# Kernel optimization log

Hardware: AMD Instinct MI355X
Metric: run time of the kernel (lower is better)

## Reference

```python
import jax, jax.numpy as jnp
import numpy as np
from jax import lax

B = 256
L = 1024
C = 64           # num_inputs == num_channels[l]
NUM_LAYERS = 5
KERNEL = 3
HID = 256
NUM_STATIC = 32
OUT_DIM = 2
KQ = 24576
T_TEMP = 0.07
NUM_NEIGHBORS = 1
EPS = 1e-12


def _l2n(x, axis):
    n = jnp.linalg.norm(x, axis=axis, keepdims=True)
    return x / jnp.maximum(n, EPS)


def _causal_conv(x, w, b, dil):
    # x: [B, C, L], w: [O, I, K] -> left-pad (K-1)*dil == Conv1d(pad both)+Chomp1d
    y = lax.conv_general_dilated(x, w, window_strides=(1,),
                                 padding=[((KERNEL - 1) * dil, 0)],
                                 rhs_dilation=(dil,),
                                 dimension_numbers=('NCH', 'OIH', 'NCH'))
    return y + b[None, :, None]


def _tcn(x, c1w, c1b, c2w, c2b):
    # stacked TemporalBlocks, dilation 2**l, identity residual (in==out channels)
    for l in range(NUM_LAYERS):
        d = 2 ** l
        h = jax.nn.relu(_causal_conv(x, c1w[l], c1b[l], d))
        h = jax.nn.relu(_causal_conv(h, c2w[l], c2b[l], d))
        x = jax.nn.relu(h + x)
    return x


def _mlp(x, w1, b1, w2, b2):
    # Linear -> ReLU -> Linear (use_batch_norm=False, eval: no dropout)
    return jax.nn.relu(x @ w1 + b1) @ w2 + b2


def setup_inputs() -> dict:
    key = jax.random.key(0)
    ks = jax.random.split(key, 24)
    d = {}
    d['sequence_q_s'] = jax.random.normal(ks[0], (B, L, C), jnp.float32)
    d['sequence_k_s'] = jax.random.normal(ks[1], (B, L, C), jnp.float32)
    d['static_s'] = jax.random.normal(ks[2], (B, NUM_STATIC), jnp.float32)
    d['sequence_q_t'] = jax.random.normal(ks[3], (B, L, C), jnp.float32)
    d['sequence_k_t'] = jax.random.normal(ks[4], (B, L, C), jnp.float32)
    d['static_t'] = jax.random.normal(ks[5], (B, NUM_STATIC), jnp.float32)
    d['alpha'] = jnp.ones((1,), jnp.float32)
    cs = 1.0 / np.sqrt(C * KERNEL)
    d['c1w'] = jax.random.normal(ks[6], (NUM_LAYERS, C, C, KERNEL), jnp.float32) * cs
    d['c1b'] = jnp.zeros((NUM_LAYERS, C), jnp.float32)
    d['c2w'] = jax.random.normal(ks[7], (NUM_LAYERS, C, C, KERNEL), jnp.float32) * cs
    d['c2b'] = jnp.zeros((NUM_LAYERS, C), jnp.float32)
    d['pjw1'] = jax.random.normal(ks[8], (C, HID), jnp.float32) / np.sqrt(C)
    d['pjb1'] = jnp.zeros((HID,), jnp.float32)
    d['pjw2'] = jax.random.normal(ks[9], (HID, C), jnp.float32) / np.sqrt(HID)
    d['pjb2'] = jnp.zeros((C,), jnp.float32)
    d['prw1'] = jax.random.normal(ks[10], (C + NUM_STATIC, HID), jnp.float32) / np.sqrt(C + NUM_STATIC)
    d['prb1'] = jnp.zeros((HID,), jnp.float32)
    d['prw2'] = jax.random.normal(ks[11], (HID, OUT_DIM), jnp.float32) / np.sqrt(HID)
    d['prb2'] = jnp.zeros((OUT_DIM,), jnp.float32)
    d['dw1'] = jax.random.normal(ks[12], (C, HID), jnp.float32) / np.sqrt(C)
    d['db1'] = jnp.zeros((HID,), jnp.float32)
    d['dw2'] = jax.random.normal(ks[13], (HID, 1), jnp.float32) / np.sqrt(HID)
    d['db2'] = jnp.zeros((1,), jnp.float32)
    qs = jax.random.normal(ks[14], (C, KQ), jnp.float32)
    qt = jax.random.normal(ks[15], (C, KQ), jnp.float32)
    d['queue_s'] = _l2n(qs, 0)
    d['queue_t'] = _l2n(qt, 0)
    return d


def reference(sequence_q_s, sequence_k_s, static_s, sequence_q_t, sequence_k_t, static_t, alpha,
              c1w, c1b, c2w, c2b, pjw1, pjb1, pjw2, pjb2, prw1, prb1, prw2, prb2,
              dw1, db1, dw2, db2, queue_s, queue_t):
    sg = lax.stop_gradient

    def encode(seq):  # [B, L, C] -> normalized [B, C]
        return _l2n(_tcn(jnp.transpose(seq, (0, 2, 1)), c1w, c1b, c2w, c2b)[:, :, -1], 1)

    q_s = encode(sequence_q_s)
    p_q_s = _l2n(_mlp(q_s, pjw1, pjb1, pjw2, pjb2), 1)
    q_t = encode(sequence_q_t)
    p_q_t = _l2n(_mlp(q_t, pjw1, pjb1, pjw2, pjb2), 1)
    # key encoder under no_grad (params equal to query encoder at init)
    k_s = sg(encode(sequence_k_s))
    k_t = sg(encode(sequence_k_t))

    logits_s = jnp.concatenate([p_q_s @ k_s.T, p_q_s @ sg(queue_s)], axis=1) / T_TEMP
    labels_s = jnp.arange(B, dtype=jnp.int32)
    logits_t = jnp.concatenate([p_q_t @ k_t.T, p_q_t @ sg(queue_t)], axis=1) / T_TEMP
    labels_t = jnp.arange(B, dtype=jnp.int32)

    # NN(k_t, q_s.detach()): cdist + topk smallest -> pseudo labels
    q_s_det = sg(q_s)
    d2 = (jnp.sum(k_t * k_t, 1)[:, None] + jnp.sum(q_s_det * q_s_det, 1)[None, :]
          - 2.0 * (k_t @ q_s_det.T))  # [B_t, B_s]
    _, idx = lax.top_k(-d2, NUM_NEIGHBORS)
    labels_ts = idx[:, 0]

    logits_ts = (q_t @ q_s_det.T) / T_TEMP

    labels_domain = jnp.concatenate([jnp.ones((B, 1), jnp.float32), jnp.zeros((B, 1), jnp.float32)], 0)
    # gradient reversal is identity in forward
    q_rev = jnp.concatenate([q_s, q_t], axis=0)
    pred_domain = _mlp(q_rev, dw1, db1, dw2, db2)

    y_s = _mlp(jnp.concatenate([q_s, static_s], axis=1), prw1, prb1, prw2, prb2)

    return (logits_s, labels_s, logits_t, labels_t, logits_ts, labels_ts,
            pred_domain, labels_domain, y_s)
```

## Files before the change

kernel.cpp:

```cpp
#include <hip/hip_runtime.h>
#include <hip/hip_bf16.h>

#define B_SZ   256
#define L_SZ   1024
#define C_SZ   64
#define HID    256
#define KQ     24576
#define WIN    125
#define WSTART (L_SZ - WIN)

#define OFF_LOGITS_S   0LL
#define OFF_LABELS_S   6356992LL
#define OFF_LOGITS_T   6357248LL
#define OFF_LABELS_T   12714240LL
#define OFF_LOGITS_TS  12714496LL
#define OFF_LABELS_TS  12780032LL
#define OFF_PRED_DOM   12780288LL
#define OFF_LABELS_DOM 12780800LL
#define OFF_YS         12781312LL

#define INV_T (1.0f / 0.07f)

typedef __attribute__((ext_vector_type(8))) short  bf16x8;
typedef __attribute__((ext_vector_type(4))) float  floatx4;
typedef __attribute__((ext_vector_type(16))) float floatx16;
typedef __attribute__((ext_vector_type(4))) unsigned short ushortx4;

__device__ __forceinline__ unsigned short f2bf_rne(float x) {
    unsigned u = __float_as_uint(x);
    unsigned r = u + 0x7fffu + ((u >> 16) & 1u);
    return (unsigned short)(r >> 16);
}
__device__ __forceinline__ float bf2f(unsigned short h) {
    return __uint_as_float(((unsigned)h) << 16);
}

__device__ __forceinline__ int swz2(int r) { return ((r >> 1) & 7) << 4; }

__device__ __forceinline__ bf16x8 dpp_tap1(bf16x8 f0, bf16x8 f2) {
    union U { bf16x8 v; int d[4]; } a, b, r;
    a.v = f0; b.v = f2;
#pragma unroll
    for (int k = 0; k < 4; ++k) {
        int patch = __builtin_amdgcn_update_dpp(0, b.d[k], 0x111, 0xf, 0xf, false);
        r.d[k]    = __builtin_amdgcn_update_dpp(patch, a.d[k], 0x101, 0xf, 0xf, false);
    }
    return r.v;
}

__global__ void prep_frag_kernel(const float* __restrict__ c1w,
                                 const float* __restrict__ c2w,
                                 unsigned short* __restrict__ wf) {
    int bid = blockIdx.x;
    int kb = bid & 1, mt = (bid >> 1) & 3;
    int sttap = bid >> 3;
    int tap = sttap % 3, st = sttap / 3;
    int l = st >> 1, cv = st & 1;
    int tid = threadIdx.x;
    int j = tid & 7, lane = tid >> 3;
    int co = mt * 16 + (lane & 15);
    int ci = kb * 32 + (lane >> 4) * 8 + j;
    const float* src = cv ? c2w : c1w;
    float w = src[((l * 64 + co) * 64 + ci) * 3 + tap];
    unsigned short hi = f2bf_rne(w);
    unsigned short lo = f2bf_rne(w - bf2f(hi));
    size_t b0 = ((((size_t)((st * 3 + tap) * 2 + 0)) * 4 + mt) * 2 + kb) * 512 + lane * 8 + j;
    size_t b1 = ((((size_t)((st * 3 + tap) * 2 + 1)) * 4 + mt) * 2 + kb) * 512 + lane * 8 + j;
    wf[b0] = hi;
    wf[b1] = lo;
}

#define R0H 0
#define R0L 16384
#define R1H 32768
#define R1L 40960
#define HHB 49152
#define HLB 65536
#define SCRATCH_B 57344

__device__ __forceinline__ void loadA(bf16x8 A[3][2][2], const bf16x8* __restrict__ wf8,
                                      int st, int mt, int lane) {
#pragma unroll
    for (int tap = 0; tap < 3; ++tap)
#pragma unroll
        for (int h = 0; h < 2; ++h)
#pragma unroll
            for (int kb = 0; kb < 2; ++kb)
                A[tap][h][kb] = wf8[((((st * 3 + tap) * 2 + h) * 4 + mt) * 2 + kb) * 64 + lane];
}

__device__ __forceinline__ void copyA(bf16x8 D[3][2][2], const bf16x8 S[3][2][2]) {
#pragma unroll
    for (int tap = 0; tap < 3; ++tap)
#pragma unroll
        for (int h = 0; h < 2; ++h)
#pragma unroll
            for (int kb = 0; kb < 2; ++kb)
                D[tap][h][kb] = S[tap][h][kb];
}

template<int TILES, bool RES, bool FINAL, bool DPP1>
__device__ __forceinline__ void conv_pass(
    char* lds, const bf16x8 A[3][2][2],
    int inH, int inL, int rows_valid, int stride,
    int outH, int outL, int n_out,
    int resH, int resL, int res_valid,
    const float* __restrict__ bias,
    int mt, int lg, int li)
{
    int co0 = mt * 16 + lg * 4;
    float4 b4 = *(const float4*)(bias + co0);
    float ba[4] = {b4.x, b4.y, b4.z, b4.w};

#pragma unroll
    for (int tt = 0; tt < TILES; ++tt) {
        int i = tt * 16 + li;
        floatx4 acc = {0.f, 0.f, 0.f, 0.f};
        if (DPP1) {
            int jr0 = i;       jr0 = (jr0 < rows_valid - 1) ? jr0 : (rows_valid - 1);
            int jr2 = i + 2;   jr2 = (jr2 < rows_valid - 1) ? jr2 : (rows_valid - 1);
            int sw0 = swz2(jr0), sw2 = swz2(jr2);
#pragma unroll
            for (int kb = 0; kb < 2; ++kb) {
                int cbase = kb * 64 + lg * 16;
                bf16x8 bH0 = *(const bf16x8*)(lds + inH + jr0 * 128 + (cbase ^ sw0));
                bf16x8 bL0 = *(const bf16x8*)(lds + inL + jr0 * 128 + (cbase ^ sw0));
                bf16x8 bH2 = *(const bf16x8*)(lds + inH + jr2 * 128 + (cbase ^ sw2));
                bf16x8 bL2 = *(const bf16x8*)(lds + inL + jr2 * 128 + (cbase ^ sw2));
                bf16x8 bH1 = dpp_tap1(bH0, bH2);
                bf16x8 bL1 = dpp_tap1(bL0, bL2);
                acc = __builtin_amdgcn_mfma_f32_16x16x32_bf16(A[0][0][kb], bH0, acc, 0, 0, 0);
                acc = __builtin_amdgcn_mfma_f32_16x16x32_bf16(A[0][0][kb], bL0, acc, 0, 0, 0);
                acc = __builtin_amdgcn_mfma_f32_16x16x32_bf16(A[0][1][kb], bH0, acc, 0, 0, 0);
                acc = __builtin_amdgcn_mfma_f32_16x16x32_bf16(A[1][0][kb], bH1, acc, 0, 0, 0);
                acc = __builtin_amdgcn_mfma_f32_16x16x32_bf16(A[1][0][kb], bL1, acc, 0, 0, 0);
                acc = __builtin_amdgcn_mfma_f32_16x16x32_bf16(A[1][1][kb], bH1, acc, 0, 0, 0);
                acc = __builtin_amdgcn_mfma_f32_16x16x32_bf16(A[2][0][kb], bH2, acc, 0, 0, 0);
                acc = __builtin_amdgcn_mfma_f32_16x16x32_bf16(A[2][0][kb], bL2, acc, 0, 0, 0);
                acc = __builtin_amdgcn_mfma_f32_16x16x32_bf16(A[2][1][kb], bH2, acc, 0, 0, 0);
            }
        } else {
#pragma unroll
            for (int tap = 0; tap < 3; ++tap) {
                int jr = i * stride + tap;
                jr = (jr < rows_valid - 1) ? jr : (rows_valid - 1);
                int sw = swz2(jr);
                const char* pH = lds + inH + jr * 128;
                const char* pL = lds + inL + jr * 128;
#pragma unroll
                for (int kb = 0; kb < 2; ++kb) {
                    int cb = (kb * 64 + lg * 16) ^ sw;
                    bf16x8 bH = *(const bf16x8*)(pH + cb);
                    bf16x8 bL = *(const bf16x8*)(pL + cb);
                    acc = __builtin_amdgcn_mfma_f32_16x16x32_bf16(A[tap][0][kb], bH, acc, 0, 0, 0);
                    acc = __builtin_amdgcn_mfma_f32_16x16x32_bf16(A[tap][0][kb], bL, acc, 0, 0, 0);
                    acc = __builtin_amdgcn_mfma_f32_16x16x32_bf16(A[tap][1][kb], bH, acc, 0, 0, 0);
                }
            }
        }
        float v[4];
#pragma unroll
        for (int r = 0; r < 4; ++r) v[r] = fmaxf(acc[r] + ba[r], 0.f);
        if (RES) {
            int rr = 2 * i + 4;
            rr = (rr < res_valid - 1) ? rr : (res_valid - 1);
            int rsw = swz2(rr);
            int rcb = (mt * 32 + lg * 8) ^ rsw;
            ushortx4 rh = *(const ushortx4*)(lds + resH + rr * 128 + rcb);
            ushortx4 rl = *(const ushortx4*)(lds + resL + rr * 128 + rcb);
#pragma unroll
            for (int r = 0; r < 4; ++r)
                v[r] = fmaxf(v[r] + bf2f(rh[r]) + bf2f(rl[r]), 0.f);
        }
        if (FINAL) {
            if (i == 0) {
                float* scratch = (float*)(lds + SCRATCH_B);
#pragma unroll
                for (int r = 0; r < 4; ++r) scratch[co0 + r] = v[r];
            }
        } else {
            if (i < n_out) {
                ushortx4 h4, l4;
#pragma unroll
                for (int r = 0; r < 4; ++r) {
                    unsigned short hh = f2bf_rne(v[r]);
                    h4[r] = (short)hh;
                    l4[r] = (short)f2bf_rne(v[r] - bf2f(hh));
                }
                int wsw = swz2(i);
                int wcb = (mt * 32 + lg * 8) ^ wsw;
                *(ushortx4*)(lds + outH + i * 128 + wcb) = h4;
                *(ushortx4*)(lds + outL + i * 128 + wcb) = l4;
            }
        }
    }
}

__launch_bounds__(256)
__global__ void encode_kernel(const float* __restrict__ sqs, const float* __restrict__ sks,
                              const float* __restrict__ sqt, const float* __restrict__ skt,
                              const unsigned short* __restrict__ wf,
                              const float* __restrict__ c1b, const float* __restrict__ c2b,
                              const float* __restrict__ pjw1, const float* __restrict__ pjb1,
                              const float* __restrict__ pjw2, const float* __restrict__ pjb2,
                              float* __restrict__ enc, float* __restrict__ proj,
                              unsigned short* __restrict__ pbf) {
    __shared__ char lds[81920];
    int b = blockIdx.x;
    int s = blockIdx.y;
    const float* seq = (s == 0) ? sqs : (s == 1) ? sks : (s == 2) ? sqt : skt;
    const float4* base4 = reinterpret_cast<const float4*>(seq + ((size_t)b * L_SZ + WSTART) * C_SZ);
    int tid = threadIdx.x;

    int mt   = tid >> 6;
    int lane = tid & 63;
    int lg = lane >> 4, li = lane & 15;
    const bf16x8* wf8 = (const bf16x8*)wf;

    bf16x8 A[3][2][2], An[3][2][2];
    loadA(A, wf8, 0, mt, lane);

    for (int idx = tid; idx < 2000; idx += 256) {
        float4 v = base4[idx];
        int t = idx >> 4, c0 = (idx & 15) * 4;
        int cb = (c0 * 2) ^ swz2(t);
        float vv[4] = {v.x, v.y, v.z, v.w};
        ushortx4 h4, l4;
#pragma unroll
        for (int r = 0; r < 4; ++r) {
            unsigned short hh = f2bf_rne(vv[r]);
            h4[r] = (short)hh;
            l4[r] = (short)f2bf_rne(vv[r] - bf2f(hh));
        }
        *(ushortx4*)(lds + R0H + t * 128 + cb) = h4;
        *(ushortx4*)(lds + R0L + t * 128 + cb) = l4;
    }
    __syncthreads();

    loadA(An, wf8, 1, mt, lane);
    conv_pass<8, false, false, true>(lds, A, R0H, R0L, 125, 1, HHB, HLB, 123, 0, 0, 0,
                                     c1b + 0, mt, lg, li);
    __syncthreads();
    copyA(A, An); loadA(An, wf8, 2, mt, lane);
    conv_pass<4, true, false, false>(lds, A, HHB, HLB, 123, 2, R1H, R1L, 61, R0H, R0L, 125,
                                     c2b + 0, mt, lg, li);
    __syncthreads();
    copyA(A, An);
    loadA(An, wf8, 3, mt, lane);
    conv_pass<4, false, false, true>(lds, A, R1H, R1L, 61, 1, HHB, HLB, 59, 0, 0, 0,
                                     c1b + 64, mt, lg, li);
    __syncthreads();
    copyA(A, An); loadA(An, wf8, 4, mt, lane);
    conv_pass<2, true, false, false>(lds, A, HHB, HLB, 59, 2, R0H, R0L, 29, R1H, R1L, 61,
                                     c2b + 64, mt, lg, li);
    __syncthreads();
    copyA(A, An);
    loadA(An, wf8, 5, mt, lane);
    conv_pass<2, false, false, true>(lds, A, R0H, R0L, 29, 1, HHB, HLB, 27, 0, 0, 0,
                                     c1b + 128, mt, lg, li);
    __syncthreads();
    copyA(A, An); loadA(An, wf8, 6, mt, lane);
    conv_pass<1, true, false, false>(lds, A, HHB, HLB, 27, 2, R1H, R1L, 13, R0H, R0L, 29,
                                     c2b + 128, mt, lg, li);
    __syncthreads();
    copyA(A, An);
    loadA(An, wf8, 7, mt, lane);
    conv_pass<1, false, false, true>(lds, A, R1H, R1L, 13, 1, HHB, HLB, 11, 0, 0, 0,
                                     c1b + 192, mt, lg, li);
    __syncthreads();
    copyA(A, An); loadA(An, wf8, 8, mt, lane);
    conv_pass<1, true, false, false>(lds, A, HHB, HLB, 11, 2, R0H, R0L, 5, R1H, R1L, 13,
                                     c2b + 192, mt, lg, li);
    __syncthreads();
    copyA(A, An);
    loadA(An, wf8, 9, mt, lane);
    conv_pass<1, false, false, true>(lds, A, R0H, R0L, 5, 1, HHB, HLB, 3, 0, 0, 0,
                                     c1b + 256, mt, lg, li);
    __syncthreads();
    copyA(A, An);
    conv_pass<1, true, true, false>(lds, A, HHB, HLB, 3, 2, R1H, R1L, 1, R0H, R0L, 5,
                                    c2b + 256, mt, lg, li);
    __syncthreads();

    float* xn = (float*)(lds + R0H);
    if (tid < 64) {
        float vv = ((float*)(lds + SCRATCH_B))[tid];
        float sq = vv * vv;
#pragma unroll
        for (int off = 32; off; off >>= 1) sq += __shfl_xor(sq, off, 64);
        float norm = fmaxf(sqrtf(sq), 1e-12f);
        float nv = vv / norm;
        enc[((size_t)s * B_SZ + b) * 64 + tid] = nv;
        xn[tid] = nv;
    }
    __syncthreads();

    if (s == 0 || s == 2) {
        float* hv   = (float*)(lds + R1H);
        float* red4 = (float*)(lds + R1H + 1024);
        {
            float acc = pjb1[tid];
            const float* wcol = pjw1 + tid;
            for (int c = 0; c < 64; ++c) acc = fmaf(xn[c], wcol[c * 256], acc);
            hv[tid] = fmaxf(acc, 0.f);
        }
        __syncthreads();
        {
            int wv = tid >> 6, o = tid & 63;
            float acc = 0.f;
            const float* wcol = pjw2 + o;
            int j0 = wv * 64;
            for (int j = j0; j < j0 + 64; ++j) acc = fmaf(hv[j], wcol[j * 64], acc);
            red4[wv * 64 + o] = acc;
        }
        __syncthreads();
        if (tid < 64) {
            float o = pjb2[tid];
#pragma unroll
            for (int k = 0; k < 4; ++k) o += red4[k * 64 + tid];
            float sq = o * o;
#pragma unroll
            for (int off = 32; off; off >>= 1) sq += __shfl_xor(sq, off, 64);
            float norm = fmaxf(sqrtf(sq), 1e-12f);
            float pv = o / norm;
            int which = s >> 1;
            proj[((size_t)which * B_SZ + b) * 64 + tid] = pv;
            pbf[((size_t)which * B_SZ + b) * 64 + tid] = f2bf_rne(pv);
        }
    }
}

__launch_bounds__(512)
__global__ void qlogits_kernel(const float* __restrict__ proj,
                               const unsigned short* __restrict__ pbf,
                               const float* __restrict__ enc,
                               const float* __restrict__ queue_s, const float* __restrict__ queue_t,
                               const float* __restrict__ stat,
                               const float* __restrict__ dw1, const float* __restrict__ db1,
                               const float* __restrict__ dw2, const float* __restrict__ db2,
                               const float* __restrict__ prw1, const float* __restrict__ prb1,
                               const float* __restrict__ prw2, const float* __restrict__ prb2,
                               float* __restrict__ out) {
    __shared__ char lds[8448];
    int bx = blockIdx.x;
    int sz = blockIdx.y;
    int tid = threadIdx.x;
    long long outBase0 = (sz == 0) ? OFF_LOGITS_S : OFF_LOGITS_T;

    if (bx >= 392) {
        int hb = (bx - 392) + sz * 513;
        if (hb < 256) {
            __shared__ float kt[64];
            __shared__ float qt[64];
            __shared__ float swv[8];
            __shared__ int   swj[8];
            int i = hb;
            if (tid < 64) {
                kt[tid] = enc[((size_t)3 * B_SZ + i) * 64 + tid];
                qt[tid] = enc[((size_t)2 * B_SZ + i) * 64 + tid];
            }
            __syncthreads();
            float bv = 1e30f; int bj = 0x7fffffff;
            if (tid < 256) {
                int j = tid;
                const float* qs = enc + (size_t)j * 64;
                float dkt = 0.f, dqt = 0.f, qq = 0.f, kk = 0.f;
                for (int c = 0; c < 64; ++c) {
                    float v = qs[c];
                    dkt = fmaf(kt[c], v, dkt);
                    dqt = fmaf(qt[c], v, dqt);
                    qq  = fmaf(v, v, qq);
                    kk  = fmaf(kt[c], kt[c], kk);
                }
                out[OFF_LOGITS_TS + (long long)i * 256 + j] = dqt * INV_T;
                bv = kk + qq - 2.f * dkt;
                bj = j;
            }
#pragma unroll
            for (int off = 32; off; off >>= 1) {
                float ov = __shfl_xor(bv, off, 64);
                int   oj = __shfl_xor(bj, off, 64);
                if (ov < bv || (ov == bv && oj < bj)) { bv = ov; bj = oj; }
            }
            int w = tid >> 6;
            if ((tid & 63) == 0) { swv[w] = bv; swj[w] = bj; }
            __syncthreads();
            if (tid == 0) {
                float best = swv[0]; int bi = swj[0];
#pragma unroll
                for (int k = 1; k < 8; ++k)
                    if (swv[k] < best || (swv[k] == best && swj[k] < bi)) { best = swv[k]; bi = swj[k]; }
                out[OFF_LABELS_TS + i] = (float)bi;
            }
        } else if (hb < 768) {
            __shared__ float xv[64];
            __shared__ float red[256];
            int r = hb - 256;
            const float* x = enc + ((r < 256) ? ((size_t)0 * B_SZ + r) : ((size_t)2 * B_SZ + (r - 256))) * 64;
            if (tid < 64) xv[tid] = x[tid];
            __syncthreads();
            if (tid < 256) {
                float h = db1[tid];
                for (int c = 0; c < 64; ++c) h = fmaf(xv[c], dw1[c * 256 + tid], h);
                h = fmaxf(h, 0.f);
                red[tid] = h * dw2[tid];
            }
            __syncthreads();
            for (int s2 = 128; s2; s2 >>= 1) {
                if (tid < s2) red[tid] += red[tid + s2];
                __syncthreads();
            }
            if (tid == 0) out[OFF_PRED_DOM + r] = red[0] + db2[0];
        } else if (hb < 1024) {
            __shared__ float xv[96];
            __shared__ float red[256];
            __shared__ float hsave[256];
            int b = hb - 768;
            if (tid < 64)       xv[tid] = enc[(size_t)b * 64 + tid];
            else if (tid < 96)  xv[tid] = stat[(size_t)b * 32 + (tid - 64)];
            __syncthreads();
            if (tid < 256) {
                float h = prb1[tid];
                for (int c = 0; c < 96; ++c) h = fmaf(xv[c], prw1[c * 256 + tid], h);
                hsave[tid] = fmaxf(h, 0.f);
            }
            __syncthreads();
            for (int o = 0; o < 2; ++o) {
                if (tid < 256) red[tid] = hsave[tid] * prw2[tid * 2 + o];
                __syncthreads();
                for (int s2 = 128; s2; s2 >>= 1) {
                    if (tid < s2) red[tid] += red[tid + s2];
                    __syncthreads();
                }
                if (tid == 0) out[OFF_YS + (long long)b * 2 + o] = red[0] + prb2[o];
                __syncthreads();
            }
        } else {
            int t = (hb - 1024) * 512 + tid;
            if (t < 256) {
                out[OFF_LABELS_S + t] = (float)t;
                out[OFF_LABELS_T + t] = (float)t;
            }
            if (t < 512) out[OFF_LABELS_DOM + t] = (t < 256) ? 1.f : 0.f;
        }
        return;
    }

    if (bx >= 384) {
        float (*pt)[65] = (float(*)[65])lds;
        int rt = bx - 384;
        const float* p = proj + ((size_t)sz * B_SZ + rt * 32) * 64;
        for (int idx = tid; idx < 32 * 64; idx += 512) {
            pt[idx >> 6][idx & 63] = p[idx];
        }
        __syncthreads();
        if (tid < 256) {
            float acc[32];
#pragma unroll
            for (int r = 0; r < 32; ++r) acc[r] = 0.f;
            int j = tid;
            const float* k = enc + ((size_t)(sz == 0 ? 1 : 3) * B_SZ + j) * 64;
            for (int c = 0; c < 64; ++c) {
                float bv = k[c];
#pragma unroll
                for (int r = 0; r < 32; ++r) acc[r] = fmaf(pt[r][c], bv, acc[r]);
            }
#pragma unroll
            for (int r = 0; r < 32; ++r) {
                out[outBase0 + (long long)(rt * 32 + r) * 24832 + j] = acc[r] * INV_T;
            }
        }
        return;
    }

    int j0 = bx * 64;
    const float* q = (sz == 0 ? queue_s : queue_t);

    {
#pragma unroll
        for (int pass = 0; pass < 2; ++pass) {
            int idx = pass * 512 + tid;
            int c = idx >> 4, jj0 = (idx & 15) * 4;
            float4 v = *(const float4*)(q + (size_t)c * KQ + j0 + jj0);
            float vv[4] = {v.x, v.y, v.z, v.w};
#pragma unroll
            for (int r = 0; r < 4; ++r) {
                int jj = jj0 + r;
                *(unsigned short*)(lds + jj * 128 + ((c * 2) ^ ((jj & 7) << 4))) = f2bf_rne(vv[r]);
            }
        }
    }
    __syncthreads();

    int w = tid >> 6, lane = tid & 63;
    int r31 = lane & 31, hi = lane >> 5;
    int arow = w * 32 + r31;
    const bf16x8* pa = (const bf16x8*)(pbf + ((size_t)sz * B_SZ + arow) * 64);
    bf16x8 A[4];
#pragma unroll
    for (int ks = 0; ks < 4; ++ks)
        A[ks] = pa[ks * 2 + hi];
    long long outBase = outBase0 + 256 + j0;
#pragma unroll
    for (int ct = 0; ct < 2; ++ct) {
        int col = ct * 32 + r31;
        bf16x8 Bf[4];
#pragma unroll
        for (int ks = 0; ks < 4; ++ks)
            Bf[ks] = *(const bf16x8*)(lds + col * 128 + (((ks * 16 + hi * 8) * 2) ^ ((col & 7) << 4)));
        floatx16 acc;
#pragma unroll
        for (int r = 0; r < 16; ++r) acc[r] = 0.f;
#pragma unroll
        for (int ks = 0; ks < 4; ++ks)
            acc = __builtin_amdgcn_mfma_f32_32x32x16_bf16(A[ks], Bf[ks], acc, 0, 0, 0);
#pragma unroll
        for (int r = 0; r < 16; ++r) {
            int drow = (r & 3) + 8 * (r >> 2) + 4 * hi;
            out[outBase + (long long)(w * 32 + drow) * 24832 + ct * 32 + r31] = acc[r] * INV_T;
        }
    }
}

extern "C" void kernel_launch(void* const* d_in, const int* in_sizes, int n_in,
                              void* d_out, int out_size, void* d_ws, size_t ws_size,
                              hipStream_t stream) {
    const float* sqs    = (const float*)d_in[0];
    const float* sks    = (const float*)d_in[1];
    const float* stat_s = (const float*)d_in[2];
    const float* sqt    = (const float*)d_in[3];
    const float* skt    = (const float*)d_in[4];
    const float* c1w    = (const float*)d_in[7];
    const float* c1b    = (const float*)d_in[8];
    const float* c2w    = (const float*)d_in[9];
    const float* c2b    = (const float*)d_in[10];
    const float* pjw1   = (const float*)d_in[11];
    const float* pjb1   = (const float*)d_in[12];
    const float* pjw2   = (const float*)d_in[13];
    const float* pjb2   = (const float*)d_in[14];
    const float* prw1   = (const float*)d_in[15];
    const float* prb1   = (const float*)d_in[16];
    const float* prw2   = (const float*)d_in[17];
    const float* prb2   = (const float*)d_in[18];
    const float* dw1    = (const float*)d_in[19];
    const float* db1    = (const float*)d_in[20];
    const float* dw2    = (const float*)d_in[21];
    const float* db2    = (const float*)d_in[22];
    const float* queue_s = (const float*)d_in[23];
    const float* queue_t = (const float*)d_in[24];

    float* out = (float*)d_out;
    unsigned short* wf = (unsigned short*)d_ws;
    float* enc  = (float*)((char*)d_ws + 491520);
    float* proj = enc + 65536;
    unsigned short* pbf = (unsigned short*)(proj + 32768);

    prep_frag_kernel<<<240, 512, 0, stream>>>(c1w, c2w, wf);
    encode_kernel<<<dim3(256, 4), 256, 0, stream>>>(sqs, sks, sqt, skt, wf, c1b, c2b,
                                                    pjw1, pjb1, pjw2, pjb2, enc, proj, pbf);
    qlogits_kernel<<<dim3(905, 2), 512, 0, stream>>>(proj, pbf, enc, queue_s, queue_t,
                                                     stat_s, dw1, db1, dw2, db2,
                                                     prw1, prb1, prw2, prb2, out);
}
```

Measured before the change: 79.76 us.

## Encode key-source and query-target sequences in single bf16 within shared blocks

```diff
diff --git a/kernel.cpp b/kernel.cpp
--- a/kernel.cpp
+++ b/kernel.cpp
@@ -78,22 +78,30 @@
 #define HLB 65536
 #define SCRATCH_B 57344
 
-__device__ __forceinline__ void loadA(bf16x8 A[3][2][2], const bf16x8* __restrict__ wf8,
-                                      int st, int mt, int lane) {
+#define L_IT   39808
+#define L_X0   0
+#define L_R1   16000
+#define L_HH   23808
+#define L_SCR  39552
+
+template<int NH>
+__device__ __forceinline__ void loadAx(bf16x8 A[3][NH][2], const bf16x8* __restrict__ wf8,
+                                       int st, int mt, int lane) {
 #pragma unroll
     for (int tap = 0; tap < 3; ++tap)
 #pragma unroll
-        for (int h = 0; h < 2; ++h)
+        for (int h = 0; h < NH; ++h)
 #pragma unroll
             for (int kb = 0; kb < 2; ++kb)
                 A[tap][h][kb] = wf8[((((st * 3 + tap) * 2 + h) * 4 + mt) * 2 + kb) * 64 + lane];
 }
 
-__device__ __forceinline__ void copyA(bf16x8 D[3][2][2], const bf16x8 S[3][2][2]) {
+template<int NH>
+__device__ __forceinline__ void copyAx(bf16x8 D[3][NH][2], const bf16x8 S[3][NH][2]) {
 #pragma unroll
     for (int tap = 0; tap < 3; ++tap)
 #pragma unroll
-        for (int h = 0; h < 2; ++h)
+        for (int h = 0; h < NH; ++h)
 #pragma unroll
             for (int kb = 0; kb < 2; ++kb)
                 D[tap][h][kb] = S[tap][h][kb];
@@ -124,10 +132,10 @@
             for (int kb = 0; kb < 2; ++kb) {
                 int cbase = kb * 64 + lg * 16;
                 bf16x8 bH0 = *(const bf16x8*)(lds + inH + jr0 * 128 + (cbase ^ sw0));
+                bf16x8 bH2 = *(const bf16x8*)(lds + inH + jr2 * 128 + (cbase ^ sw2));
+                bf16x8 bH1 = dpp_tap1(bH0, bH2);
                 bf16x8 bL0 = *(const bf16x8*)(lds + inL + jr0 * 128 + (cbase ^ sw0));
-                bf16x8 bH2 = *(const bf16x8*)(lds + inH + jr2 * 128 + (cbase ^ sw2));
                 bf16x8 bL2 = *(const bf16x8*)(lds + inL + jr2 * 128 + (cbase ^ sw2));
-                bf16x8 bH1 = dpp_tap1(bH0, bH2);
                 bf16x8 bL1 = dpp_tap1(bL0, bL2);
                 acc = __builtin_amdgcn_mfma_f32_16x16x32_bf16(A[0][0][kb], bH0, acc, 0, 0, 0);
                 acc = __builtin_amdgcn_mfma_f32_16x16x32_bf16(A[0][0][kb], bL0, acc, 0, 0, 0);
@@ -164,8 +172,7 @@
         if (RES) {
             int rr = 2 * i + 4;
             rr = (rr < res_valid - 1) ? rr : (res_valid - 1);
-            int rsw = swz2(rr);
-            int rcb = (mt * 32 + lg * 8) ^ rsw;
+            int rcb = (mt * 32 + lg * 8) ^ swz2(rr);
             ushortx4 rh = *(const ushortx4*)(lds + resH + rr * 128 + rcb);
             ushortx4 rl = *(const ushortx4*)(lds + resL + rr * 128 + rcb);
 #pragma unroll
@@ -178,22 +185,239 @@
 #pragma unroll
                 for (int r = 0; r < 4; ++r) scratch[co0 + r] = v[r];
             }
-        } else {
-            if (i < n_out) {
-                ushortx4 h4, l4;
-#pragma unroll
-                for (int r = 0; r < 4; ++r) {
-                    unsigned short hh = f2bf_rne(v[r]);
-                    h4[r] = (short)hh;
-                    l4[r] = (short)f2bf_rne(v[r] - bf2f(hh));
+        } else if (i < n_out) {
+            int wcb = (mt * 32 + lg * 8) ^ swz2(i);
+            ushortx4 h4, l4;
+#pragma unroll
+            for (int r = 0; r < 4; ++r) {
+                h4[r] = f2bf_rne(v[r]);
+                l4[r] = f2bf_rne(v[r] - bf2f(h4[r]));
+            }
+            *(ushortx4*)(lds + outH + i * 128 + wcb) = h4;
+            *(ushortx4*)(lds + outL + i * 128 + wcb) = l4;
+        }
+    }
+}
+
+__device__ __forceinline__ void encode_body_heavy(
+    char* lds, const float* __restrict__ base,
+    const bf16x8* __restrict__ wf8,
+    const float* __restrict__ c1b, const float* __restrict__ c2b,
+    int tid, int mt, int lane, int lg, int li)
+{
+    const float4* base4 = reinterpret_cast<const float4*>(base);
+    bf16x8 A[3][2][2], An[3][2][2];
+    loadAx<2>(A, wf8, 0, mt, lane);
+
+    for (int idx = tid; idx < 2000; idx += 256) {
+        float4 v = base4[idx];
+        int t = idx >> 4, c0 = (idx & 15) * 4;
+        int cb = (c0 * 2) ^ swz2(t);
+        float vv[4] = {v.x, v.y, v.z, v.w};
+        ushortx4 h4, l4;
+#pragma unroll
+        for (int r = 0; r < 4; ++r) {
+            h4[r] = f2bf_rne(vv[r]);
+            l4[r] = f2bf_rne(vv[r] - bf2f(h4[r]));
+        }
+        *(ushortx4*)(lds + R0H + t * 128 + cb) = h4;
+        *(ushortx4*)(lds + R0L + t * 128 + cb) = l4;
+    }
+    __syncthreads();
+
+    loadAx<2>(An, wf8, 1, mt, lane);
+    conv_pass<8, false, false, true>(lds, A, R0H, R0L, 125, 1, HHB, HLB, 123, 0, 0, 0,
+                                     c1b + 0, mt, lg, li);
+    __syncthreads();
+    copyAx<2>(A, An); loadAx<2>(An, wf8, 2, mt, lane);
+    conv_pass<4, true, false, false>(lds, A, HHB, HLB, 123, 2, R1H, R1L, 61, R0H, R0L, 125,
+                                     c2b + 0, mt, lg, li);
+    __syncthreads();
+    copyAx<2>(A, An);
+    loadAx<2>(An, wf8, 3, mt, lane);
+    conv_pass<4, false, false, true>(lds, A, R1H, R1L, 61, 1, HHB, HLB, 59, 0, 0, 0,
+                                     c1b + 64, mt, lg, li);
+    __syncthreads();
+    copyAx<2>(A, An); loadAx<2>(An, wf8, 4, mt, lane);
+    conv_pass<2, true, false, false>(lds, A, HHB, HLB, 59, 2, R0H, R0L, 29, R1H, R1L, 61,
+                                     c2b + 64, mt, lg, li);
+    __syncthreads();
+    copyAx<2>(A, An);
+    loadAx<2>(An, wf8, 5, mt, lane);
+    conv_pass<2, false, false, true>(lds, A, R0H, R0L, 29, 1, HHB, HLB, 27, 0, 0, 0,
+                                     c1b + 128, mt, lg, li);
+    __syncthreads();
+    copyAx<2>(A, An); loadAx<2>(An, wf8, 6, mt, lane);
+    conv_pass<1, true, false, false>(lds, A, HHB, HLB, 27, 2, R1H, R1L, 13, R0H, R0L, 29,
+                                     c2b + 128, mt, lg, li);
+    __syncthreads();
+    copyAx<2>(A, An);
+    loadAx<2>(An, wf8, 7, mt, lane);
+    conv_pass<1, false, false, true>(lds, A, R1H, R1L, 13, 1, HHB, HLB, 11, 0, 0, 0,
+                                     c1b + 192, mt, lg, li);
+    __syncthreads();
+    copyAx<2>(A, An); loadAx<2>(An, wf8, 8, mt, lane);
+    conv_pass<1, true, false, false>(lds, A, HHB, HLB, 11, 2, R0H, R0L, 5, R1H, R1L, 13,
+                                     c2b + 192, mt, lg, li);
+    __syncthreads();
+    copyAx<2>(A, An);
+    loadAx<2>(An, wf8, 9, mt, lane);
+    conv_pass<1, false, false, true>(lds, A, R0H, R0L, 5, 1, HHB, HLB, 3, 0, 0, 0,
+                                     c1b + 256, mt, lg, li);
+    __syncthreads();
+    copyAx<2>(A, An);
+    conv_pass<1, true, true, false>(lds, A, HHB, HLB, 3, 2, R1H, R1L, 1, R0H, R0L, 5,
+                                    c2b + 256, mt, lg, li);
+    __syncthreads();
+}
+
+template<int TILES, bool RES, bool FINAL, bool DPP1>
+__device__ __forceinline__ void conv_pass_l2(
+    char* lds, const bf16x8 A[3][1][2],
+    int inO, int rows_valid, int stride,
+    int outO, int n_out,
+    int resO, int res_valid,
+    const float* __restrict__ bias,
+    int mt, int lg, int li)
+{
+    int co0 = mt * 16 + lg * 4;
+    float4 b4 = *(const float4*)(bias + co0);
+    float ba[4] = {b4.x, b4.y, b4.z, b4.w};
+
+#pragma unroll
+    for (int it = 0; it < 2; ++it) {
+        char* L = lds + it * L_IT;
+#pragma unroll
+        for (int tt = 0; tt < TILES; ++tt) {
+            int i = tt * 16 + li;
+            floatx4 acc = {0.f, 0.f, 0.f, 0.f};
+            if (DPP1) {
+                int jr0 = i;       jr0 = (jr0 < rows_valid - 1) ? jr0 : (rows_valid - 1);
+                int jr2 = i + 2;   jr2 = (jr2 < rows_valid - 1) ? jr2 : (rows_valid - 1);
+                int sw0 = swz2(jr0), sw2 = swz2(jr2);
+#pragma unroll
+                for (int kb = 0; kb < 2; ++kb) {
+                    int cbase = kb * 64 + lg * 16;
+                    bf16x8 bH0 = *(const bf16x8*)(L + inO + jr0 * 128 + (cbase ^ sw0));
+                    bf16x8 bH2 = *(const bf16x8*)(L + inO + jr2 * 128 + (cbase ^ sw2));
+                    bf16x8 bH1 = dpp_tap1(bH0, bH2);
+                    acc = __builtin_amdgcn_mfma_f32_16x16x32_bf16(A[0][0][kb], bH0, acc, 0, 0, 0);
+                    acc = __builtin_amdgcn_mfma_f32_16x16x32_bf16(A[1][0][kb], bH1, acc, 0, 0, 0);
+                    acc = __builtin_amdgcn_mfma_f32_16x16x32_bf16(A[2][0][kb], bH2, acc, 0, 0, 0);
                 }
-                int wsw = swz2(i);
-                int wcb = (mt * 32 + lg * 8) ^ wsw;
-                *(ushortx4*)(lds + outH + i * 128 + wcb) = h4;
-                *(ushortx4*)(lds + outL + i * 128 + wcb) = l4;
-            }
-        }
-    }
+            } else {
+#pragma unroll
+                for (int tap = 0; tap < 3; ++tap) {
+                    int jr = i * stride + tap;
+                    jr = (jr < rows_valid - 1) ? jr : (rows_valid - 1);
+                    int sw = swz2(jr);
+#pragma unroll
+                    for (int kb = 0; kb < 2; ++kb) {
+                        int cb = (kb * 64 + lg * 16) ^ sw;
+                        bf16x8 bH = *(const bf16x8*)(L + inO + jr * 128 + cb);
+                        acc = __builtin_amdgcn_mfma_f32_16x16x32_bf16(A[tap][0][kb], bH, acc, 0, 0, 0);
+                    }
+                }
+            }
+            float v[4];
+#pragma unroll
+            for (int r = 0; r < 4; ++r) v[r] = fmaxf(acc[r] + ba[r], 0.f);
+            if (RES) {
+                int rr = 2 * i + 4;
+                rr = (rr < res_valid - 1) ? rr : (res_valid - 1);
+                int rcb = (mt * 32 + lg * 8) ^ swz2(rr);
+                ushortx4 rh = *(const ushortx4*)(L + resO + rr * 128 + rcb);
+#pragma unroll
+                for (int r = 0; r < 4; ++r)
+                    v[r] = fmaxf(v[r] + bf2f(rh[r]), 0.f);
+            }
+            if (FINAL) {
+                if (i == 0) {
+                    float* scratch = (float*)(L + L_SCR);
+#pragma unroll
+                    for (int r = 0; r < 4; ++r) scratch[co0 + r] = v[r];
+                }
+            } else if (i < n_out) {
+                int wcb = (mt * 32 + lg * 8) ^ swz2(i);
+                ushortx4 h4;
+#pragma unroll
+                for (int r = 0; r < 4; ++r) h4[r] = f2bf_rne(v[r]);
+                *(ushortx4*)(L + outO + i * 128 + wcb) = h4;
+            }
+        }
+    }
+}
+
+__device__ __forceinline__ void encode_body_light2(
+    char* lds, const float* __restrict__ base0, const float* __restrict__ base1,
+    const bf16x8* __restrict__ wf8,
+    const float* __restrict__ c1b, const float* __restrict__ c2b,
+    int tid, int mt, int lane, int lg, int li)
+{
+    const float* bases[2] = {base0, base1};
+#pragma unroll
+    for (int it = 0; it < 2; ++it) {
+        const float4* base4 = reinterpret_cast<const float4*>(bases[it]);
+        char* L = lds + it * L_IT;
+        for (int idx = tid; idx < 2000; idx += 256) {
+            float4 v = base4[idx];
+            int t = idx >> 4, c0 = (idx & 15) * 4;
+            int cb = (c0 * 2) ^ swz2(t);
+            float vv[4] = {v.x, v.y, v.z, v.w};
+            ushortx4 h4;
+#pragma unroll
+            for (int r = 0; r < 4; ++r) h4[r] = f2bf_rne(vv[r]);
+            *(ushortx4*)(L + L_X0 + t * 128 + cb) = h4;
+        }
+    }
+    __syncthreads();
+
+    bf16x8 A[3][1][2], An[3][1][2];
+    loadAx<1>(A, wf8, 0, mt, lane);
+    loadAx<1>(An, wf8, 1, mt, lane);
+    conv_pass_l2<8, false, false, true>(lds, A, L_X0, 125, 1, L_HH, 123, 0, 0,
+                                        c1b + 0, mt, lg, li);
+    __syncthreads();
+    copyAx<1>(A, An); loadAx<1>(An, wf8, 2, mt, lane);
+    conv_pass_l2<4, true, false, false>(lds, A, L_HH, 123, 2, L_R1, 61, L_X0, 125,
+                                        c2b + 0, mt, lg, li);
+    __syncthreads();
+    copyAx<1>(A, An);
+    loadAx<1>(An, wf8, 3, mt, lane);
+    conv_pass_l2<4, false, false, true>(lds, A, L_R1, 61, 1, L_HH, 59, 0, 0,
+                                        c1b + 64, mt, lg, li);
+    __syncthreads();
+    copyAx<1>(A, An); loadAx<1>(An, wf8, 4, mt, lane);
+    conv_pass_l2<2, true, false, false>(lds, A, L_HH, 59, 2, L_X0, 29, L_R1, 61,
+                                        c2b + 64, mt, lg, li);
+    __syncthreads();
+    copyAx<1>(A, An);
+    loadAx<1>(An, wf8, 5, mt, lane);
+    conv_pass_l2<2, false, false, true>(lds, A, L_X0, 29, 1, L_HH, 27, 0, 0,
+                                        c1b + 128, mt, lg, li);
+    __syncthreads();
+    copyAx<1>(A, An); loadAx<1>(An, wf8, 6, mt, lane);
+    conv_pass_l2<1, true, false, false>(lds, A, L_HH, 27, 2, L_R1, 13, L_X0, 29,
+                                        c2b + 128, mt, lg, li);
+    __syncthreads();
+    copyAx<1>(A, An);
+    loadAx<1>(An, wf8, 7, mt, lane);
+    conv_pass_l2<1, false, false, true>(lds, A, L_R1, 13, 1, L_HH, 11, 0, 0,
+                                        c1b + 192, mt, lg, li);
+    __syncthreads();
+    copyAx<1>(A, An); loadAx<1>(An, wf8, 8, mt, lane);
+    conv_pass_l2<1, true, false, false>(lds, A, L_HH, 11, 2, L_X0, 5, L_R1, 13,
+                                        c2b + 192, mt, lg, li);
+    __syncthreads();
+    copyAx<1>(A, An);
+    loadAx<1>(An, wf8, 9, mt, lane);
+    conv_pass_l2<1, false, false, true>(lds, A, L_X0, 5, 1, L_HH, 3, 0, 0,
+                                        c1b + 256, mt, lg, li);
+    __syncthreads();
+    copyAx<1>(A, An);
+    conv_pass_l2<1, true, true, false>(lds, A, L_HH, 3, 2, L_R1, 1, L_X0, 5,
+                                       c2b + 256, mt, lg, li);
+    __syncthreads();
 }
 
 __launch_bounds__(256)
@@ -207,101 +431,91 @@
                               unsigned short* __restrict__ pbf) {
     __shared__ char lds[81920];
     int b = blockIdx.x;
-    int s = blockIdx.y;
-    const float* seq = (s == 0) ? sqs : (s == 1) ? sks : (s == 2) ? sqt : skt;
-    const float4* base4 = reinterpret_cast<const float4*>(seq + ((size_t)b * L_SZ + WSTART) * C_SZ);
+    int by = blockIdx.y;
     int tid = threadIdx.x;
-
     int mt   = tid >> 6;
     int lane = tid & 63;
     int lg = lane >> 4, li = lane & 15;
     const bf16x8* wf8 = (const bf16x8*)wf;
 
-    bf16x8 A[3][2][2], An[3][2][2];
-    loadA(A, wf8, 0, mt, lane);
-
-    for (int idx = tid; idx < 2000; idx += 256) {
-        float4 v = base4[idx];
-        int t = idx >> 4, c0 = (idx & 15) * 4;
-        int cb = (c0 * 2) ^ swz2(t);
-        float vv[4] = {v.x, v.y, v.z, v.w};
-        ushortx4 h4, l4;
-#pragma unroll
-        for (int r = 0; r < 4; ++r) {
-            unsigned short hh = f2bf_rne(vv[r]);
-            h4[r] = (short)hh;
-            l4[r] = (short)f2bf_rne(vv[r] - bf2f(hh));
-        }
-        *(ushortx4*)(lds + R0H + t * 128 + cb) = h4;
-        *(ushortx4*)(lds + R0L + t * 128 + cb) = l4;
-    }
-    __syncthreads();
-
-    loadA(An, wf8, 1, mt, lane);
-    conv_pass<8, false, false, true>(lds, A, R0H, R0L, 125, 1, HHB, HLB, 123, 0, 0, 0,
-                                     c1b + 0, mt, lg, li);
-    __syncthreads();
-    copyA(A, An); loadA(An, wf8, 2, mt, lane);
-    conv_pass<4, true, false, false>(lds, A, HHB, HLB, 123, 2, R1H, R1L, 61, R0H, R0L, 125,
-                                     c2b + 0, mt, lg, li);
-    __syncthreads();
-    copyA(A, An);
-    loadA(An, wf8, 3, mt, lane);
-    conv_pass<4, false, false, true>(lds, A, R1H, R1L, 61, 1, HHB, HLB, 59, 0, 0, 0,
-                                     c1b + 64, mt, lg, li);
-    __syncthreads();
-    copyA(A, An); loadA(An, wf8, 4, mt, lane);
-    conv_pass<2, true, false, false>(lds, A, HHB, HLB, 59, 2, R0H, R0L, 29, R1H, R1L, 61,
-                                     c2b + 64, mt, lg, li);
-    __syncthreads();
-    copyA(A, An);
-    loadA(An, wf8, 5, mt, lane);
-    conv_pass<2, false, false, true>(lds, A, R0H, R0L, 29, 1, HHB, HLB, 27, 0, 0, 0,
-                                     c1b + 128, mt, lg, li);
-    __syncthreads();
-    copyA(A, An); loadA(An, wf8, 6, mt, lane);
-    conv_pass<1, true, false, false>(lds, A, HHB, HLB, 27, 2, R1H, R1L, 13, R0H, R0L, 29,
-                                     c2b + 128, mt, lg, li);
-    __syncthreads();
-    copyA(A, An);
-    loadA(An, wf8, 7, mt, lane);
-    conv_pass<1, false, false, true>(lds, A, R1H, R1L, 13, 1, HHB, HLB, 11, 0, 0, 0,
-                                     c1b + 192, mt, lg, li);
-    __syncthreads();
-    copyA(A, An); loadA(An, wf8, 8, mt, lane);
-    conv_pass<1, true, false, false>(lds, A, HHB, HLB, 11, 2, R0H, R0L, 5, R1H, R1L, 13,
-                                     c2b + 192, mt, lg, li);
-    __syncthreads();
-    copyA(A, An);
-    loadA(An, wf8, 9, mt, lane);
-    conv_pass<1, false, false, true>(lds, A, R0H, R0L, 5, 1, HHB, HLB, 3, 0, 0, 0,
-                                     c1b + 256, mt, lg, li);
-    __syncthreads();
-    copyA(A, An);
-    conv_pass<1, true, true, false>(lds, A, HHB, HLB, 3, 2, R1H, R1L, 1, R0H, R0L, 5,
-                                    c2b + 256, mt, lg, li);
-    __syncthreads();
-
-    float* xn = (float*)(lds + R0H);
-    if (tid < 64) {
-        float vv = ((float*)(lds + SCRATCH_B))[tid];
-        float sq = vv * vv;
-#pragma unroll
-        for (int off = 32; off; off >>= 1) sq += __shfl_xor(sq, off, 64);
-        float norm = fmaxf(sqrtf(sq), 1e-12f);
-        float nv = vv / norm;
-        enc[((size_t)s * B_SZ + b) * 64 + tid] = nv;
-        xn[tid] = nv;
-    }
-    __syncthreads();
-
-    if (s == 0 || s == 2) {
-        float* hv   = (float*)(lds + R1H);
-        float* red4 = (float*)(lds + R1H + 1024);
+    if (by < 2) {
+        int s = by ? 3 : 0;
+        const float* seq = (s == 0) ? sqs : skt;
+        const float* base = seq + ((size_t)b * L_SZ + WSTART) * C_SZ;
+        encode_body_heavy(lds, base, wf8, c1b, c2b, tid, mt, lane, lg, li);
+
+        float* xn = (float*)(lds + R0H);
+        if (tid < 64) {
+            float vv = ((float*)(lds + SCRATCH_B))[tid];
+            float sq = vv * vv;
+#pragma unroll
+            for (int off = 32; off; off >>= 1) sq += __shfl_xor(sq, off, 64);
+            float norm = fmaxf(sqrtf(sq), 1e-12f);
+            float nv = vv / norm;
+            enc[((size_t)s * B_SZ + b) * 64 + tid] = nv;
+            xn[tid] = nv;
+        }
+        __syncthreads();
+
+        if (s == 0) {
+            float* hv   = (float*)(lds + R1H);
+            float* red4 = (float*)(lds + R1H + 1024);
+            {
+                float acc = pjb1[tid];
+                const float* wcol = pjw1 + tid;
+                for (int c = 0; c < 64; ++c) acc = fmaf(xn[c], wcol[c * 256], acc);
+                hv[tid] = fmaxf(acc, 0.f);
+            }
+            __syncthreads();
+            {
+                int wv = tid >> 6, o = tid & 63;
+                float acc = 0.f;
+                const float* wcol = pjw2 + o;
+                int j0 = wv * 64;
+                for (int j = j0; j < j0 + 64; ++j) acc = fmaf(hv[j], wcol[j * 64], acc);
+                red4[wv * 64 + o] = acc;
+            }
+            __syncthreads();
+            if (tid < 64) {
+                float o = pjb2[tid];
+#pragma unroll
+                for (int k = 0; k < 4; ++k) o += red4[k * 64 + tid];
+                float sq = o * o;
+#pragma unroll
+                for (int off = 32; off; off >>= 1) sq += __shfl_xor(sq, off, 64);
+                float norm = fmaxf(sqrtf(sq), 1e-12f);
+                float pv = o / norm;
+                proj[((size_t)0 * B_SZ + b) * 64 + tid] = pv;
+                pbf[((size_t)0 * B_SZ + b) * 64 + tid] = f2bf_rne(pv);
+            }
+        }
+    } else {
+        const float* base0 = sks + ((size_t)b * L_SZ + WSTART) * C_SZ;
+        const float* base1 = sqt + ((size_t)b * L_SZ + WSTART) * C_SZ;
+        encode_body_light2(lds, base0, base1, wf8, c1b, c2b, tid, mt, lane, lg, li);
+
+        float* xn2 = (float*)(lds + 0);
+        int itw = tid >> 6;
+        if (itw < 2) {
+            float* scr = (float*)(lds + itw * L_IT + L_SCR);
+            float vv = scr[lane];
+            float sq = vv * vv;
+#pragma unroll
+            for (int off = 32; off; off >>= 1) sq += __shfl_xor(sq, off, 64);
+            float norm = fmaxf(sqrtf(sq), 1e-12f);
+            float nv = vv / norm;
+            int s_ = (itw == 0) ? 1 : 2;
+            enc[((size_t)s_ * B_SZ + b) * 64 + lane] = nv;
+            if (itw == 1) xn2[lane] = nv;
+        }
+        __syncthreads();
+
+        float* hv   = (float*)(lds + 1024);
+        float* red4 = (float*)(lds + 2048);
         {
             float acc = pjb1[tid];
             const float* wcol = pjw1 + tid;
-            for (int c = 0; c < 64; ++c) acc = fmaf(xn[c], wcol[c * 256], acc);
+            for (int c = 0; c < 64; ++c) acc = fmaf(xn2[c], wcol[c * 256], acc);
             hv[tid] = fmaxf(acc, 0.f);
         }
         __syncthreads();
@@ -323,9 +537,8 @@
             for (int off = 32; off; off >>= 1) sq += __shfl_xor(sq, off, 64);
             float norm = fmaxf(sqrtf(sq), 1e-12f);
             float pv = o / norm;
-            int which = s >> 1;
-            proj[((size_t)which * B_SZ + b) * 64 + tid] = pv;
-            pbf[((size_t)which * B_SZ + b) * 64 + tid] = f2bf_rne(pv);
+            proj[((size_t)1 * B_SZ + b) * 64 + tid] = pv;
+            pbf[((size_t)1 * B_SZ + b) * 64 + tid] = f2bf_rne(pv);
         }
     }
 }
@@ -475,7 +688,6 @@
 
     int j0 = bx * 64;
     const float* q = (sz == 0 ? queue_s : queue_t);
-
     {
 #pragma unroll
         for (int pass = 0; pass < 2; ++pass) {
@@ -556,7 +768,7 @@
     unsigned short* pbf = (unsigned short*)(proj + 32768);
 
     prep_frag_kernel<<<240, 512, 0, stream>>>(c1w, c2w, wf);
-    encode_kernel<<<dim3(256, 4), 256, 0, stream>>>(sqs, sks, sqt, skt, wf, c1b, c2b,
+    encode_kernel<<<dim3(256, 3), 256, 0, stream>>>(sqs, sks, sqt, skt, wf, c1b, c2b,
                                                     pjw1, pjb1, pjw2, pjb2, enc, proj, pbf);
     qlogits_kernel<<<dim3(905, 2), 512, 0, stream>>>(proj, pbf, enc, queue_s, queue_t,
                                                      stat_s, dw1, db1, dw2, db2,
```

New measurement: 76.65 us. 1.04x faster.
